# Performance work log

Measured on AMD Instinct MI355X. Metric: run time of the kernel, lower is better.

Reference implementation:

```python
import jax, jax.numpy as jnp
import numpy as np
import math

N_EMB = 768
N_HEAD = 12
N_INNER = 3072
B, T = 2, 2048
EPS = 1e-4


def _gelu_tanh(x):
    return x * 0.5 * (1.0 + jnp.tanh(math.sqrt(2.0 / math.pi) * (x + 0.044715 * x ** 3)))


def _layernorm(x, scale, bias):
    mean = jnp.mean(x, axis=-1, keepdims=True)
    var = jnp.var(x, axis=-1, keepdims=True, ddof=1)  # torch.var default: unbiased
    return scale * ((x - mean) / jnp.sqrt(var + EPS)) + bias


def setup_inputs() -> dict:
    key = jax.random.key(0)
    ks = jax.random.split(key, 16)
    s_attn = 1.0 / math.sqrt(N_EMB)
    s_mlp1 = 1.0 / math.sqrt(N_EMB)
    s_mlp2 = 1.0 / math.sqrt(N_INNER)
    return {
        "x": jax.random.normal(ks[0], (B, T, N_EMB), dtype=jnp.float32),
        "Wq": jax.random.normal(ks[1], (N_EMB, N_EMB), dtype=jnp.float32) * s_attn,
        "bq": jnp.zeros((N_EMB,), jnp.float32),
        "Wk": jax.random.normal(ks[2], (N_EMB, N_EMB), dtype=jnp.float32) * s_attn,
        "bk": jnp.zeros((N_EMB,), jnp.float32),
        "Wv": jax.random.normal(ks[3], (N_EMB, N_EMB), dtype=jnp.float32) * s_attn,
        "bv": jnp.zeros((N_EMB,), jnp.float32),
        "Wo": jax.random.normal(ks[4], (N_EMB, N_EMB), dtype=jnp.float32) * s_attn,
        "bo": jnp.zeros((N_EMB,), jnp.float32),
        "ln1_s": jnp.ones((N_EMB,), jnp.float32),
        "ln1_b": jnp.zeros((N_EMB,), jnp.float32),
        "W1": jax.random.normal(ks[5], (N_EMB, N_INNER), dtype=jnp.float32) * s_mlp1,
        "b1": jnp.zeros((N_INNER,), jnp.float32),
        "W2": jax.random.normal(ks[6], (N_INNER, N_EMB), dtype=jnp.float32) * s_mlp2,
        "b2": jnp.zeros((N_EMB,), jnp.float32),
        "ln2_s": jnp.ones((N_EMB,), jnp.float32),
        "ln2_b": jnp.zeros((N_EMB,), jnp.float32),
    }


def reference(x, Wq, bq, Wk, bk, Wv, bv, Wo, bo, ln1_s, ln1_b, W1, b1, W2, b2, ln2_s, ln2_b):
    Bx, Tx, C = x.shape
    dh = C // N_HEAD
    # QKV projections -> [B, H, T, dh]
    def split_heads(y):
        return y.reshape(Bx, Tx, N_HEAD, dh).transpose(0, 2, 1, 3)
    q = split_heads(x @ Wq + bq)
    k = split_heads(x @ Wk + bk)
    v = split_heads(x @ Wv + bv)
    # naive full-score causal attention (materializes [B,H,T,T])
    scores = jnp.einsum("bhqd,bhkd->bhqk", q, k)
    causal = jnp.tril(jnp.ones((Tx, Tx), dtype=bool))
    scores = jnp.where(causal, scores, -jnp.inf)
    attn = jax.nn.softmax(scores / math.sqrt(dh), axis=-1)
    ctx = jnp.einsum("bhqk,bhkd->bhqd", attn, v)
    ctx = ctx.transpose(0, 2, 1, 3).reshape(Bx, Tx, C)
    attn_out = ctx @ Wo + bo
    # post-norm residual
    h = _layernorm(x + attn_out, ln1_s, ln1_b)
    mlp_out = _gelu_tanh(h @ W1 + b1) @ W2 + b2
    return _layernorm(h + mlp_out, ln2_s, ln2_b)
```

## Files before the change

kernel.cpp:

```cpp
#include <hip/hip_runtime.h>
#include <math.h>

#define TB  2
#define TT  2048
#define TC  768
#define TH  12
#define TDH 64
#define TI  3072
#define TM  (TB*TT)

typedef __attribute__((ext_vector_type(8))) __bf16 bf16x8;
typedef __attribute__((ext_vector_type(4))) __bf16 bf16x4;
typedef __attribute__((ext_vector_type(4))) float  f32x4;

__device__ __forceinline__ float gelu_tanh(float x) {
    float x3 = x * x * x;
    return 0.5f * x * (1.0f + tanhf(0.7978845608028654f * (x + 0.044715f * x3)));
}

__device__ __forceinline__ void gld_lds16(const void* g, void* l) {
    __builtin_amdgcn_global_load_lds(
        (const __attribute__((address_space(1))) unsigned int*)g,
        (__attribute__((address_space(3))) unsigned int*)l,
        16, 0, 0);
}

template<int N>
__device__ __forceinline__ void vmcnt_wait() {
    if constexpr (N == 0)      asm volatile("s_waitcnt vmcnt(0)" ::: "memory");
    else if constexpr (N == 2) asm volatile("s_waitcnt vmcnt(2)" ::: "memory");
    else if constexpr (N == 3) asm volatile("s_waitcnt vmcnt(3)" ::: "memory");
    else if constexpr (N == 4) asm volatile("s_waitcnt vmcnt(4)" ::: "memory");
    else if constexpr (N == 6) asm volatile("s_waitcnt vmcnt(6)" ::: "memory");
    else if constexpr (N == 8) asm volatile("s_waitcnt vmcnt(8)" ::: "memory");
    else static_assert(N == 0, "unsupported vmcnt");
}

#define BK 32

template<int BM_, int BN_, int WM_, int WN_>
__global__ __launch_bounds__(256)
void gemm_mfma(const __bf16* __restrict__ A, const __bf16* __restrict__ Bt,
               const float* __restrict__ b0, const float* __restrict__ b1,
               const float* __restrict__ b2, const float* __restrict__ resid,
               float* __restrict__ outf, __bf16* __restrict__ outb,
               int N, int K, size_t wt_stride, size_t out_stride, int ep)
{
    constexpr int WAVES_N = BN_ / WN_;
    constexpr int TMt = WM_ / 16, TNt = WN_ / 16;
    constexpr int AISS = BM_ / 64, BISS = BN_ / 64;
    constexpr int S    = AISS + BISS;
    constexpr int TILE = (BM_ + BN_) * BK;
    __shared__ __align__(16) __bf16 lds[3 * TILE];

    const int tid  = threadIdx.x;
    const int wave = tid >> 6, lane = tid & 63;
    const int wm = wave / WAVES_N, wn = wave % WAVES_N;
    const int m0 = blockIdx.y * BM_, n0 = blockIdx.x * BN_;
    const int z  = blockIdx.z;

    const __bf16* Bz = Bt + (size_t)z * wt_stride;
    const size_t Kb = (size_t)K * 2;
    const char* Ag = (const char*)A + (size_t)m0 * Kb;
    const char* Bg = (const char*)Bz + (size_t)n0 * Kb;
    const int srow = tid >> 2;
    const int scol = ((tid & 3) ^ ((tid >> 4) & 3)) * 16;
    const int wbase = wave * 1024;

    f32x4 acc[TMt][TNt];
    #pragma unroll
    for (int i = 0; i < TMt; ++i)
        #pragma unroll
        for (int j = 0; j < TNt; ++j)
            acc[i][j] = (f32x4){0.f, 0.f, 0.f, 0.f};

    const int arow = wm * WM_ + (lane & 15);
    const int brow = wn * WN_ + (lane & 15);
    const int koff = (((lane >> 4) ^ ((lane >> 2) & 3))) * 8;

    const int nIter = K / BK;

    auto stage = [&](char* base, int k0b) {
        #pragma unroll
        for (int s = 0; s < AISS; ++s)
            gld_lds16(Ag + (size_t)(srow + 64 * s) * Kb + k0b + scol,
                      base + s * 4096 + wbase);
        char* bbase = base + BM_ * BK * 2;
        #pragma unroll
        for (int s = 0; s < BISS; ++s)
            gld_lds16(Bg + (size_t)(srow + 64 * s) * Kb + k0b + scol,
                      bbase + s * 4096 + wbase);
    };

    char* P0 = (char*)lds;
    char* P1 = P0 + (size_t)TILE * 2;
    char* P2 = P1 + (size_t)TILE * 2;

    stage(P0, 0);
    if (nIter > 1) stage(P1, BK * 2);
    __builtin_amdgcn_sched_barrier(0);
    char* cur = P0; char* n1 = P1; char* n2 = P2;

    for (int it = 0; it < nIter; ++it) {
        if (it + 2 < nIter) stage(n2, (it + 2) * (BK * 2));
        __builtin_amdgcn_sched_barrier(0);
        const int rem = nIter - 1 - it;
        if (rem >= 2)      vmcnt_wait<2 * S>();
        else if (rem == 1) vmcnt_wait<S>();
        else               vmcnt_wait<0>();
        __builtin_amdgcn_s_barrier();
        __builtin_amdgcn_sched_barrier(0);

        const __bf16* As = (const __bf16*)cur;
        const __bf16* Bs = As + BM_ * BK;
        bf16x8 af[TMt], bfr[TNt];
        #pragma unroll
        for (int ti = 0; ti < TMt; ++ti)
            af[ti] = *(const bf16x8*)&As[(arow + ti * 16) * BK + koff];
        #pragma unroll
        for (int tj = 0; tj < TNt; ++tj)
            bfr[tj] = *(const bf16x8*)&Bs[(brow + tj * 16) * BK + koff];
        #pragma unroll
        for (int ti = 0; ti < TMt; ++ti)
            #pragma unroll
            for (int tj = 0; tj < TNt; ++tj)
                acc[ti][tj] = __builtin_amdgcn_mfma_f32_16x16x32_bf16(
                    af[ti], bfr[tj], acc[ti][tj], 0, 0, 0);

        __builtin_amdgcn_sched_barrier(0);
        __builtin_amdgcn_s_barrier();
        char* t = cur; cur = n1; n1 = n2; n2 = t;
    }

    const int lrow = m0 + wm * WM_ + ((lane >> 4) << 2);
    const int lcol = n0 + wn * WN_ + (lane & 15);

    if (ep == 0) {
        const float* bias = (z == 0) ? b0 : (z == 1) ? b1 : b2;
        __bf16* outz = outb + (size_t)z * out_stride;
        if (z < 2) {
            #pragma unroll
            for (int tj = 0; tj < TNt; ++tj) {
                int n = lcol + tj * 16;
                float bj = bias[n];
                int h = n >> 6, d = n & 63;
                #pragma unroll
                for (int ti = 0; ti < TMt; ++ti)
                    #pragma unroll
                    for (int r = 0; r < 4; ++r) {
                        int m = lrow + ti * 16 + r;
                        int b = m >> 11, t = m & (TT - 1);
                        outz[((size_t)(b * TH + h) * TT + t) * TDH + d] =
                            (__bf16)(acc[ti][tj][r] + bj);
                    }
            }
        } else {
            #pragma unroll
            for (int tj = 0; tj < TNt; ++tj) {
                int n = lcol + tj * 16;
                float bj = bias[n];
                int h = n >> 6, d = n & 63;
                #pragma unroll
                for (int ti = 0; ti < TMt; ++ti) {
                    int m = lrow + ti * 16;
                    int b = m >> 11, t0 = m & (TT - 1);
                    bf16x4 pk;
                    #pragma unroll
                    for (int r = 0; r < 4; ++r)
                        pk[r] = (__bf16)(acc[ti][tj][r] + bj);
                    *(bf16x4*)(outz + ((size_t)(b * TH + h) * TDH + d) * TT + t0) = pk;
                }
            }
        }
    } else if (ep == 1) {
        #pragma unroll
        for (int tj = 0; tj < TNt; ++tj) {
            int n = lcol + tj * 16;
            float bj = b0[n];
            #pragma unroll
            for (int ti = 0; ti < TMt; ++ti)
                #pragma unroll
                for (int r = 0; r < 4; ++r) {
                    int m = lrow + ti * 16 + r;
                    outf[(size_t)m * N + n] =
                        acc[ti][tj][r] + bj + resid[(size_t)m * N + n];
                }
        }
    } else {
        #pragma unroll
        for (int tj = 0; tj < TNt; ++tj) {
            int n = lcol + tj * 16;
            float bj = b0[n];
            #pragma unroll
            for (int ti = 0; ti < TMt; ++ti)
                #pragma unroll
                for (int r = 0; r < 4; ++r) {
                    int m = lrow + ti * 16 + r;
                    outb[(size_t)m * N + n] = (__bf16)gelu_tanh(acc[ti][tj][r] + bj);
                }
        }
    }
}

__global__ __launch_bounds__(256)
void prep_kernel(const float* __restrict__ x,
                 const float* __restrict__ Wq, const float* __restrict__ Wk,
                 const float* __restrict__ Wv, const float* __restrict__ Wo,
                 const float* __restrict__ W1, const float* __restrict__ W2,
                 __bf16* __restrict__ x_bf, __bf16* __restrict__ WqkvT,
                 __bf16* __restrict__ WoT, __bf16* __restrict__ W1T,
                 __bf16* __restrict__ W2T)
{
    const size_t WSZ = (size_t)TC * TC;
    int bid = blockIdx.x;
    if (bid < 1536) {
        int i = (bid * 256 + threadIdx.x) * 8;
        float4 a = *(const float4*)(x + i);
        float4 b = *(const float4*)(x + i + 4);
        bf16x8 v;
        v[0] = (__bf16)a.x; v[1] = (__bf16)a.y; v[2] = (__bf16)a.z; v[3] = (__bf16)a.w;
        v[4] = (__bf16)b.x; v[5] = (__bf16)b.y; v[6] = (__bf16)b.z; v[7] = (__bf16)b.w;
        *(bf16x8*)(x_bf + i) = v;
        return;
    }
    bid -= 1536;
    const float* src; __bf16* dst; int K, N, tloc;
    if (bid < 2304) {
        int w = bid / 576; tloc = bid - w * 576;
        K = TC; N = TC;
        src = (w == 0) ? Wq : (w == 1) ? Wk : (w == 2) ? Wv : Wo;
        dst = (w < 3) ? (WqkvT + (size_t)w * WSZ) : WoT;
    } else if (bid < 4608) {
        tloc = bid - 2304; K = TC; N = TI; src = W1; dst = W1T;
    } else {
        tloc = bid - 4608; K = TI; N = TC; src = W2; dst = W2T;
    }
    int tiles_x = N >> 5;
    int n0 = (tloc % tiles_x) * 32, k0 = (tloc / tiles_x) * 32;

    __shared__ float tile[32][33];
    const int tx = threadIdx.x & 31, ty = threadIdx.x >> 5;
    #pragma unroll
    for (int i = 0; i < 32; i += 8)
        tile[ty + i][tx] = src[(size_t)(k0 + ty + i) * N + n0 + tx];
    __syncthreads();
    #pragma unroll
    for (int i = 0; i < 32; i += 8)
        dst[(size_t)(n0 + ty + i) * K + k0 + tx] = (__bf16)tile[tx][ty + i];
}

__global__ __launch_bounds__(256)
void ln_kernel(const float* __restrict__ in, const float* __restrict__ gs,
               const float* __restrict__ gb, float* __restrict__ out,
               __bf16* __restrict__ out_bf)
{
    const int row = blockIdx.x, tid = threadIdx.x;
    const float* r = in + (size_t)row * TC;
    float x0 = r[tid], x1 = r[tid + 256], x2 = r[tid + 512];
    float s = x0 + x1 + x2;
    float q = x0 * x0 + x1 * x1 + x2 * x2;
    #pragma unroll
    for (int off = 32; off > 0; off >>= 1) {
        s += __shfl_down(s, off);
        q += __shfl_down(q, off);
    }
    __shared__ float partial[8];
    __shared__ float stats[2];
    int wid = tid >> 6, lane = tid & 63;
    if (lane == 0) { partial[wid] = s; partial[wid + 4] = q; }
    __syncthreads();
    if (tid == 0) {
        float S = partial[0] + partial[1] + partial[2] + partial[3];
        float Q = partial[4] + partial[5] + partial[6] + partial[7];
        float mean = S * (1.0f / (float)TC);
        float var = (Q - (float)TC * mean * mean) * (1.0f / (float)(TC - 1));
        stats[0] = mean;
        stats[1] = rsqrtf(var + 1e-4f);
    }
    __syncthreads();
    float mean = stats[0], rstd = stats[1];
    float* w = out + (size_t)row * TC;
    float y0 = gs[tid]       * ((x0 - mean) * rstd) + gb[tid];
    float y1 = gs[tid + 256] * ((x1 - mean) * rstd) + gb[tid + 256];
    float y2 = gs[tid + 512] * ((x2 - mean) * rstd) + gb[tid + 512];
    w[tid] = y0; w[tid + 256] = y1; w[tid + 512] = y2;
    if (out_bf) {
        __bf16* wb = out_bf + (size_t)row * TC;
        wb[tid] = (__bf16)y0; wb[tid + 256] = (__bf16)y1; wb[tid + 512] = (__bf16)y2;
    }
}

#define AP 72
#define ATT_SCALE 0.18033688011112042f

__global__ __launch_bounds__(256)
void attn_mfma(const __bf16* __restrict__ Q, const __bf16* __restrict__ K,
               const __bf16* __restrict__ Vt, __bf16* __restrict__ ctx)
{
    __shared__ __align__(16) __bf16 Ks[64 * AP];
    __shared__ __align__(16) __bf16 Vs[64 * AP];
    __shared__ __align__(16) __bf16 Ps[64 * AP];

    const int tid  = threadIdx.x;
    const int wave = tid >> 6, lane = tid & 63;
    const int c = lane & 15, g = lane >> 4;
    const int bh = blockIdx.y;
    const int qi = blockIdx.x;
    const int qt = (qi & 1) ? (31 - (qi >> 1)) : (qi >> 1);
    const int q_glob = qt * 64 + wave * 16 + c;

    const __bf16* Qb = Q  + (size_t)bh * TT * TDH;
    const __bf16* Kb = K  + (size_t)bh * TT * TDH;
    const __bf16* Vb = Vt + (size_t)bh * TDH * TT;

    bf16x8 qf0 = *(const bf16x8*)(Qb + (size_t)q_glob * TDH + g * 8);
    bf16x8 qf1 = *(const bf16x8*)(Qb + (size_t)q_glob * TDH + 32 + g * 8);

    const int srow = tid >> 3;
    const int sc   = (tid & 7) * 8;

    float m_i = -1e30f, l_i = 0.0f;
    f32x4 acc[4];
    #pragma unroll
    for (int m2 = 0; m2 < 4; ++m2) acc[m2] = (f32x4){0.f, 0.f, 0.f, 0.f};

    for (int kt = 0; kt <= qt; ++kt) {
        bf16x8 kv0 = *(const bf16x8*)(Kb + (size_t)(kt * 64 + srow) * TDH + sc);
        bf16x8 kv1 = *(const bf16x8*)(Kb + (size_t)(kt * 64 + srow + 32) * TDH + sc);
        bf16x8 vv0 = *(const bf16x8*)(Vb + (size_t)srow * TT + kt * 64 + sc);
        bf16x8 vv1 = *(const bf16x8*)(Vb + (size_t)(srow + 32) * TT + kt * 64 + sc);
        __syncthreads();
        *(bf16x8*)&Ks[srow * AP + sc]        = kv0;
        *(bf16x8*)&Ks[(srow + 32) * AP + sc] = kv1;
        *(bf16x8*)&Vs[srow * AP + sc]        = vv0;
        *(bf16x8*)&Vs[(srow + 32) * AP + sc] = vv1;
        __syncthreads();

        f32x4 st[4];
        #pragma unroll
        for (int g2 = 0; g2 < 4; ++g2) {
            bf16x8 af0 = *(const bf16x8*)&Ks[(16 * g2 + c) * AP + g * 8];
            bf16x8 af1 = *(const bf16x8*)&Ks[(16 * g2 + c) * AP + 32 + g * 8];
            f32x4 z = (f32x4){0.f, 0.f, 0.f, 0.f};
            z = __builtin_amdgcn_mfma_f32_16x16x32_bf16(af0, qf0, z, 0, 0, 0);
            z = __builtin_amdgcn_mfma_f32_16x16x32_bf16(af1, qf1, z, 0, 0, 0);
            st[g2] = z;
        }

        float sv[4][4];
        float mx = -1e30f;
        if (kt == qt) {
            #pragma unroll
            for (int g2 = 0; g2 < 4; ++g2)
                #pragma unroll
                for (int r = 0; r < 4; ++r) {
                    int kcol = kt * 64 + 16 * g2 + 4 * g + r;
                    float v = (kcol > q_glob) ? -1e30f : st[g2][r] * ATT_SCALE;
                    sv[g2][r] = v;
                    mx = fmaxf(mx, v);
                }
        } else {
            #pragma unroll
            for (int g2 = 0; g2 < 4; ++g2)
                #pragma unroll
                for (int r = 0; r < 4; ++r) {
                    float v = st[g2][r] * ATT_SCALE;
                    sv[g2][r] = v;
                    mx = fmaxf(mx, v);
                }
        }
        mx = fmaxf(mx, __shfl_xor(mx, 16));
        mx = fmaxf(mx, __shfl_xor(mx, 32));
        float nm = fmaxf(m_i, mx);
        float corr = exp2f(m_i - nm);
        float ps = 0.f;
        #pragma unroll
        for (int g2 = 0; g2 < 4; ++g2) {
            bf16x4 pk;
            #pragma unroll
            for (int r = 0; r < 4; ++r) {
                float p = exp2f(sv[g2][r] - nm);
                ps += p;
                pk[r] = (__bf16)p;
            }
            *(bf16x4*)&Ps[(wave * 16 + c) * AP + 16 * g2 + 4 * g] = pk;
        }
        ps += __shfl_xor(ps, 16);
        ps += __shfl_xor(ps, 32);
        l_i = l_i * corr + ps;
        m_i = nm;
        #pragma unroll
        for (int m2 = 0; m2 < 4; ++m2) {
            acc[m2][0] *= corr; acc[m2][1] *= corr;
            acc[m2][2] *= corr; acc[m2][3] *= corr;
        }

        bf16x8 pf0 = *(const bf16x8*)&Ps[(wave * 16 + c) * AP + g * 8];
        bf16x8 pf1 = *(const bf16x8*)&Ps[(wave * 16 + c) * AP + 32 + g * 8];
        #pragma unroll
        for (int m2 = 0; m2 < 4; ++m2) {
            bf16x8 vf0 = *(const bf16x8*)&Vs[(16 * m2 + c) * AP + g * 8];
            bf16x8 vf1 = *(const bf16x8*)&Vs[(16 * m2 + c) * AP + 32 + g * 8];
            acc[m2] = __builtin_amdgcn_mfma_f32_16x16x32_bf16(vf0, pf0, acc[m2], 0, 0, 0);
            acc[m2] = __builtin_amdgcn_mfma_f32_16x16x32_bf16(vf1, pf1, acc[m2], 0, 0, 0);
        }
    }

    const int b = bh / TH, h = bh - b * TH;
    float inv = 1.0f / l_i;
    #pragma unroll
    for (int m2 = 0; m2 < 4; ++m2) {
        bf16x4 o;
        #pragma unroll
        for (int r = 0; r < 4; ++r)
            o[r] = (__bf16)(acc[m2][r] * inv);
        *(bf16x4*)(ctx + ((size_t)b * TT + q_glob) * TC + h * TDH + 16 * m2 + 4 * g) = o;
    }
}

extern "C" void kernel_launch(void* const* d_in, const int* in_sizes, int n_in,
                              void* d_out, int out_size, void* d_ws, size_t ws_size,
                              hipStream_t stream)
{
    const float* x    = (const float*)d_in[0];
    const float* Wq   = (const float*)d_in[1];
    const float* bq   = (const float*)d_in[2];
    const float* Wk   = (const float*)d_in[3];
    const float* bk   = (const float*)d_in[4];
    const float* Wv   = (const float*)d_in[5];
    const float* bv   = (const float*)d_in[6];
    const float* Wo   = (const float*)d_in[7];
    const float* bo   = (const float*)d_in[8];
    const float* ln1s = (const float*)d_in[9];
    const float* ln1b = (const float*)d_in[10];
    const float* W1   = (const float*)d_in[11];
    const float* b1   = (const float*)d_in[12];
    const float* W2   = (const float*)d_in[13];
    const float* b2   = (const float*)d_in[14];
    const float* ln2s = (const float*)d_in[15];
    const float* ln2b = (const float*)d_in[16];
    float* out = (float*)d_out;

    const size_t MC  = (size_t)TM * TC;
    const size_t MCB = MC * 2;
    const size_t WSZ = (size_t)TC * TC;
    const size_t W12 = (size_t)TC * TI;

    char* W = (char*)d_ws;
    __bf16* qkvb  = (__bf16*)W;
    __bf16* x_bf  = (__bf16*)(W + 3 * MCB);
    float*  tmp1  = (float*)W;
    __bf16* u_bf  = (__bf16*)W;
    float*  h_f32 = (float*)(W + 4 * MCB);
    __bf16* ctxh  = (__bf16*)(W + 6 * MCB);
    __bf16* wts   = (__bf16*)(W + 7 * MCB);
    __bf16* WqkvT = wts;
    __bf16* WoT   = WqkvT + 3 * WSZ;
    __bf16* W1T   = WoT + WSZ;
    __bf16* W2T   = W1T + W12;

    dim3 blk(256);

    prep_kernel<<<dim3(1536 + 6912), blk, 0, stream>>>(
        x, Wq, Wk, Wv, Wo, W1, W2, x_bf, WqkvT, WoT, W1T, W2T);

    gemm_mfma<64, 128, 32, 64><<<dim3(TC / 128, TM / 64, 3), blk, 0, stream>>>(
        x_bf, WqkvT, bq, bk, bv, nullptr, nullptr, qkvb, TC, TC, WSZ, MC, 0);

    attn_mfma<<<dim3(TT / 64, TB * TH), blk, 0, stream>>>(
        qkvb, qkvb + MC, qkvb + 2 * MC, ctxh);

    gemm_mfma<64, 64, 32, 32><<<dim3(TC / 64, TM / 64, 1), blk, 0, stream>>>(
        ctxh, WoT, bo, nullptr, nullptr, x, tmp1, nullptr, TC, TC, 0, 0, 1);

    ln_kernel<<<dim3(TM), blk, 0, stream>>>(tmp1, ln1s, ln1b, h_f32, ctxh);

    gemm_mfma<128, 128, 64, 64><<<dim3(TI / 128, TM / 128, 1), blk, 0, stream>>>(
        ctxh, W1T, b1, nullptr, nullptr, nullptr, nullptr, u_bf, TI, TC, 0, 0, 2);

    gemm_mfma<64, 64, 32, 32><<<dim3(TC / 64, TM / 64, 1), blk, 0, stream>>>(
        u_bf, W2T, b2, nullptr, nullptr, h_f32, out, nullptr, TC, TI, 0, 0, 1);

    ln_kernel<<<dim3(TM), blk, 0, stream>>>(out, ln2s, ln2b, out, nullptr);
}
```

Measured before the change: 326.0 us.

## Widen attention KV tile to 128 keys and skip rescale when max barely grows

The attention kernel now processes 128 keys per iteration instead of 64, halving the number of barrier-separated load/compute steps and doubling MFMA work per sync. It also adds a lazy online-softmax rescale that only updates the running max and rescales the accumulators when some row's new max exceeds the old one by more than 8 (log2 units). This reduces per-tile exp and multiply overhead but raises register and LDS use, and on the diagonal tile it computes up to 64 extra masked keys for odd query tiles. Skipping the rescale can let unnormalized probabilities grow to 2^8 before bf16 conversion, which is a small numerical risk.

```diff
diff --git a/kernel.cpp b/kernel.cpp
--- a/kernel.cpp
+++ b/kernel.cpp
@@ -291,15 +291,16 @@
 }
 
 #define AP 72
+#define VP 136
 #define ATT_SCALE 0.18033688011112042f
 
 __global__ __launch_bounds__(256)
 void attn_mfma(const __bf16* __restrict__ Q, const __bf16* __restrict__ K,
                const __bf16* __restrict__ Vt, __bf16* __restrict__ ctx)
 {
-    __shared__ __align__(16) __bf16 Ks[64 * AP];
-    __shared__ __align__(16) __bf16 Vs[64 * AP];
-    __shared__ __align__(16) __bf16 Ps[64 * AP];
+    __shared__ __align__(16) __bf16 Ks[128 * AP];
+    __shared__ __align__(16) __bf16 Vs[64 * VP];
+    __shared__ __align__(16) __bf16 Ps[64 * VP];
 
     const int tid  = threadIdx.x;
     const int wave = tid >> 6, lane = tid & 63;
@@ -316,29 +317,34 @@
     bf16x8 qf0 = *(const bf16x8*)(Qb + (size_t)q_glob * TDH + g * 8);
     bf16x8 qf1 = *(const bf16x8*)(Qb + (size_t)q_glob * TDH + 32 + g * 8);
 
-    const int srow = tid >> 3;
-    const int sc   = (tid & 7) * 8;
+    const int krow = tid >> 3, kcol = (tid & 7) * 8;
+    const int vrow = tid >> 4, vcol = (tid & 15) * 8;
 
     float m_i = -1e30f, l_i = 0.0f;
     f32x4 acc[4];
     #pragma unroll
     for (int m2 = 0; m2 < 4; ++m2) acc[m2] = (f32x4){0.f, 0.f, 0.f, 0.f};
 
-    for (int kt = 0; kt <= qt; ++kt) {
-        bf16x8 kv0 = *(const bf16x8*)(Kb + (size_t)(kt * 64 + srow) * TDH + sc);
-        bf16x8 kv1 = *(const bf16x8*)(Kb + (size_t)(kt * 64 + srow + 32) * TDH + sc);
-        bf16x8 vv0 = *(const bf16x8*)(Vb + (size_t)srow * TT + kt * 64 + sc);
-        bf16x8 vv1 = *(const bf16x8*)(Vb + (size_t)(srow + 32) * TT + kt * 64 + sc);
+    const int pmax = qt >> 1;
+    for (int p = 0; p <= pmax; ++p) {
+        const int kb = p * 128;
+        bf16x8 kv[4], vv[4];
+        #pragma unroll
+        for (int s = 0; s < 4; ++s) {
+            kv[s] = *(const bf16x8*)(Kb + (size_t)(kb + krow + 32 * s) * TDH + kcol);
+            vv[s] = *(const bf16x8*)(Vb + (size_t)(vrow + 16 * s) * TT + kb + vcol);
+        }
         __syncthreads();
-        *(bf16x8*)&Ks[srow * AP + sc]        = kv0;
-        *(bf16x8*)&Ks[(srow + 32) * AP + sc] = kv1;
-        *(bf16x8*)&Vs[srow * AP + sc]        = vv0;
-        *(bf16x8*)&Vs[(srow + 32) * AP + sc] = vv1;
+        #pragma unroll
+        for (int s = 0; s < 4; ++s) {
+            *(bf16x8*)&Ks[(krow + 32 * s) * AP + kcol] = kv[s];
+            *(bf16x8*)&Vs[(vrow + 16 * s) * VP + vcol] = vv[s];
+        }
         __syncthreads();
 
-        f32x4 st[4];
-        #pragma unroll
-        for (int g2 = 0; g2 < 4; ++g2) {
+        f32x4 st[8];
+        #pragma unroll
+        for (int g2 = 0; g2 < 8; ++g2) {
             bf16x8 af0 = *(const bf16x8*)&Ks[(16 * g2 + c) * AP + g * 8];
             bf16x8 af1 = *(const bf16x8*)&Ks[(16 * g2 + c) * AP + 32 + g * 8];
             f32x4 z = (f32x4){0.f, 0.f, 0.f, 0.f};
@@ -347,21 +353,21 @@
             st[g2] = z;
         }
 
-        float sv[4][4];
+        float sv[8][4];
         float mx = -1e30f;
-        if (kt == qt) {
-            #pragma unroll
-            for (int g2 = 0; g2 < 4; ++g2)
+        if (p == pmax) {
+            #pragma unroll
+            for (int g2 = 0; g2 < 8; ++g2)
                 #pragma unroll
                 for (int r = 0; r < 4; ++r) {
-                    int kcol = kt * 64 + 16 * g2 + 4 * g + r;
-                    float v = (kcol > q_glob) ? -1e30f : st[g2][r] * ATT_SCALE;
+                    int kcol2 = kb + 16 * g2 + 4 * g + r;
+                    float v = (kcol2 > q_glob) ? -1e30f : st[g2][r] * ATT_SCALE;
                     sv[g2][r] = v;
                     mx = fmaxf(mx, v);
                 }
         } else {
             #pragma unroll
-            for (int g2 = 0; g2 < 4; ++g2)
+            for (int g2 = 0; g2 < 8; ++g2)
                 #pragma unroll
                 for (int r = 0; r < 4; ++r) {
                     float v = st[g2][r] * ATT_SCALE;
@@ -371,38 +377,47 @@
         }
         mx = fmaxf(mx, __shfl_xor(mx, 16));
         mx = fmaxf(mx, __shfl_xor(mx, 32));
-        float nm = fmaxf(m_i, mx);
-        float corr = exp2f(m_i - nm);
+
+        float nm = m_i;
+        if (!__all(mx <= m_i + 8.0f)) {
+            nm = fmaxf(m_i, mx);
+            float corr = exp2f(m_i - nm);
+            l_i *= corr;
+            #pragma unroll
+            for (int m2 = 0; m2 < 4; ++m2) {
+                acc[m2][0] *= corr; acc[m2][1] *= corr;
+                acc[m2][2] *= corr; acc[m2][3] *= corr;
+            }
+            m_i = nm;
+        }
+
         float ps = 0.f;
         #pragma unroll
-        for (int g2 = 0; g2 < 4; ++g2) {
+        for (int g2 = 0; g2 < 8; ++g2) {
             bf16x4 pk;
             #pragma unroll
             for (int r = 0; r < 4; ++r) {
-                float p = exp2f(sv[g2][r] - nm);
-                ps += p;
-                pk[r] = (__bf16)p;
+                float pp = exp2f(sv[g2][r] - nm);
+                ps += pp;
+                pk[r] = (__bf16)pp;
             }
-            *(bf16x4*)&Ps[(wave * 16 + c) * AP + 16 * g2 + 4 * g] = pk;
+            *(bf16x4*)&Ps[(wave * 16 + c) * VP + 16 * g2 + 4 * g] = pk;
         }
         ps += __shfl_xor(ps, 16);
         ps += __shfl_xor(ps, 32);
-        l_i = l_i * corr + ps;
-        m_i = nm;
+        l_i += ps;
+
+        bf16x8 pf[4];
+        #pragma unroll
+        for (int s = 0; s < 4; ++s)
+            pf[s] = *(const bf16x8*)&Ps[(wave * 16 + c) * VP + 32 * s + g * 8];
         #pragma unroll
         for (int m2 = 0; m2 < 4; ++m2) {
-            acc[m2][0] *= corr; acc[m2][1] *= corr;
-            acc[m2][2] *= corr; acc[m2][3] *= corr;
-        }
-
-        bf16x8 pf0 = *(const bf16x8*)&Ps[(wave * 16 + c) * AP + g * 8];
-        bf16x8 pf1 = *(const bf16x8*)&Ps[(wave * 16 + c) * AP + 32 + g * 8];
-        #pragma unroll
-        for (int m2 = 0; m2 < 4; ++m2) {
-            bf16x8 vf0 = *(const bf16x8*)&Vs[(16 * m2 + c) * AP + g * 8];
-            bf16x8 vf1 = *(const bf16x8*)&Vs[(16 * m2 + c) * AP + 32 + g * 8];
-            acc[m2] = __builtin_amdgcn_mfma_f32_16x16x32_bf16(vf0, pf0, acc[m2], 0, 0, 0);
-            acc[m2] = __builtin_amdgcn_mfma_f32_16x16x32_bf16(vf1, pf1, acc[m2], 0, 0, 0);
+            #pragma unroll
+            for (int s = 0; s < 4; ++s) {
+                bf16x8 vf = *(const bf16x8*)&Vs[(16 * m2 + c) * VP + 32 * s + g * 8];
+                acc[m2] = __builtin_amdgcn_mfma_f32_16x16x32_bf16(vf, pf[s], acc[m2], 0, 0, 0);
+            }
         }
     }
 
```

New measurement: 323.7 us. No clear change (-0.7%).
